# Kernel optimization log

Measured on AMD Instinct MI355X. Metric: run time of the kernel, lower is better.

## Reference

```python
import jax, jax.numpy as jnp
import numpy as np
from jax import lax

R = 4                 # radius (init kwarg)
EPS = 2.0             # eps (init kwarg)
K = 2 * R + 1         # stencil size


def _dir_kernels():
    """8 directional box kernels [8,1,K,K]: L,R,U,D,NW,NE,SW,SE (matches torch construction)."""
    base = np.ones((K, K), np.float32)
    L = base.copy(); L[:, R + 1:] = 0
    Rk = base.copy(); Rk[:, :R] = 0
    U = base.copy(); U[R + 1:, :] = 0
    D = base.copy(); D[:R, :] = 0
    NW = U.copy(); NE = U.copy(); SW = D.copy(); SE = D.copy()
    half = float((R + 1) * (2 * R + 1))
    L, Rk, U, D = L / half, Rk / half, U / half, D / half
    NW[:, R + 1:] = 0; NE[:, :R] = 0; SW[:, R + 1:] = 0; SE[:, :R] = 0
    quad = float((R + 1) ** 2)
    NW, NE, SW, SE = NW / quad, NE / quad, SW / quad, SE / quad
    return jnp.asarray(np.stack([L, Rk, U, D, NW, NE, SW, SE])[:, None])


def _pad(x):
    # ReplicationPad2d(R)
    return jnp.pad(x, ((0, 0), (0, 0), (R, R), (R, R)), mode='edge')


def _conv(x, w, groups=1):
    return lax.conv_general_dilated(
        x, w, window_strides=(1, 1), padding='VALID',
        dimension_numbers=('NCHW', 'OIHW', 'NCHW'), feature_group_count=groups)


def _resize_bilinear_ac(x, H, W):
    """Bilinear resize with align_corners=True, separable gather. x: [N,C,h,w]."""
    n, c, h, w = x.shape
    dt = x.dtype

    def coords(out, src):
        t = jnp.arange(out, dtype=dt) * (jnp.asarray(src - 1, dt) / jnp.asarray(out - 1, dt))
        i0 = jnp.clip(jnp.floor(t).astype(jnp.int32), 0, src - 2)
        f = t - i0.astype(dt)
        return i0, f

    y0, fy = coords(H, h)
    x0, fx = coords(W, w)
    rows = x[:, :, y0, :] * (1 - fy)[None, None, :, None] + x[:, :, y0 + 1, :] * fy[None, None, :, None]
    return rows[:, :, :, x0] * (1 - fx) + rows[:, :, :, x0 + 1] * fx


def setup_inputs() -> dict:
    key = jax.random.key(0)
    k1, k2, k3 = jax.random.split(key, 3)
    lr_x = jax.random.uniform(k1, (1, 3, 256, 256), jnp.float32) * 255.0
    lr_y = jax.random.uniform(k2, (1, 3, 256, 256), jnp.float32) * 255.0
    hr_x = jax.random.uniform(k3, (1, 3, 1024, 1024), jnp.float32) * 255.0
    box_w = jnp.full((3, 1, K, K), 1.0 / (K * K), jnp.float32)  # depthwise box filter weights
    return {"lr_x": lr_x, "lr_y": lr_y, "hr_x": hr_x, "box_w": box_w}


def reference(lr_x, lr_y, hr_x, box_w):
    H, W = hr_x.shape[2], hr_x.shape[3]
    box = lambda t: _conv(_pad(t), box_w, groups=3)

    # --- guided filter coefficients at low res ---
    mean_x = box(lr_x)
    mean_y = box(lr_y)
    cov_xy = box(lr_x * lr_y) - mean_x * mean_y
    var_x = box(lr_x * lr_x) - mean_x * mean_x
    A = cov_xy / (var_x + EPS)
    b = mean_y - A * mean_x

    # --- upsample A, b to hr (bilinear, align_corners=True) ---
    A = _resize_bilinear_ac(A, H, W)
    b = _resize_bilinear_ac(b, H, W)

    # --- 8-direction side-window stencil; channels treated as batch ---
    dirw = _dir_kernels()                      # [8,1,K,K]
    A3 = _pad(A.reshape(3, 1, H, W))
    b3 = _pad(b.reshape(3, 1, H, W))
    im3 = hr_x.reshape(3, 1, H, W)
    cA = _conv(A3, dirw)                       # [3,8,H,W]
    cB = _conv(b3, dirw)                       # [3,8,H,W]
    d = cA * im3 + cB - im3                    # [3,8,H,W]

    idx = jnp.argmin(jnp.abs(d), axis=1, keepdims=True)
    dm = jnp.take_along_axis(d, idx, axis=1)   # min-|delta| direction
    res = (dm + im3).reshape(1, 3, H, W)

    # res.int() truncates toward zero, then clamp(0,255), then float
    return jnp.clip(jnp.trunc(res), 0.0, 255.0)
```

## Files before the change

kernel.cpp:

```cpp
#include <hip/hip_runtime.h>

#define LRN 256
#define HRN 1024
#define SCALE (255.0f/1023.0f)

typedef float v2 __attribute__((ext_vector_type(2)));

#define WS_LUTW 4096
#define WS_AB   65536

__device__ inline int anchor_of(int u) {
    int k = min(max(u - 4, 0), HRN - 1);
    float t = (float)k * SCALE;
    int i = (int)t; if (i > LRN - 2) i = LRN - 2;
    return i;
}

__device__ inline float4 mkw(int k0, int k1, int a) {
    float4 w = make_float4(0.f, 0.f, 0.f, 0.f);
    for (int k = k0; k <= k1; ++k) {
        int kc = min(max(k, 0), HRN - 1);
        float t = (float)kc * SCALE;
        int i = (int)t; if (i > LRN - 2) i = LRN - 2;
        float f = t - (float)i;
        int off = i - a;
        float wa = 1.0f - f, wb = f;
        w.x += (off == 0) ? wa : 0.0f;
        w.y += (off == 1) ? wa : ((off == 0) ? wb : 0.0f);
        w.z += (off == 2) ? wa : ((off == 1) ? wb : 0.0f);
        w.w += (off == 2) ? wb : 0.0f;
    }
    return w;
}

__global__ __launch_bounds__(256, 4) void lr_kernel(
    const float* __restrict__ lrx, const float* __restrict__ lry,
    float* __restrict__ ws)
{
    __shared__ float4 sV[24][40];
    __shared__ float4 sHS[24][32];

    const int c  = blockIdx.z;
    const int X0 = blockIdx.x * 32, Y0 = blockIdx.y * 16;
    const int tid = threadIdx.y * 32 + threadIdx.x;
    const float* px = lrx + c * LRN * LRN;
    const float* py = lry + c * LRN * LRN;

    if (c == 0 && blockIdx.y == 0 && tid < 128) {
        int u = blockIdx.x * 128 + tid;
        int a = anchor_of(u);
        ((int*)ws)[u] = a;
        float4* w = (float4*)((char*)ws + WS_LUTW) + u * 3;
        w[0] = mkw(u - 4, u,     a);
        w[1] = mkw(u,     u + 4, a);
        w[2] = mkw(u - 4, u + 4, a);
    }

    for (int i = tid; i < 24 * 40; i += 256) {
        int r = i / 40, cc = i - r * 40;
        int gy = min(max(Y0 - 4 + r, 0), LRN - 1);
        int gx = min(max(X0 - 4 + cc, 0), LRN - 1);
        float xv = px[gy * LRN + gx];
        float yv = py[gy * LRN + gx];
        sV[r][cc] = make_float4(xv, yv, xv * yv, xv * xv);
    }
    __syncthreads();

    for (int i = tid; i < 24 * 32; i += 256) {
        int r = i / 32, cc = i & 31;
        float4 s = sV[r][cc];
        #pragma unroll
        for (int k = 1; k < 9; ++k) {
            float4 v = sV[r][cc + k];
            s.x += v.x; s.y += v.y; s.z += v.z; s.w += v.w;
        }
        sHS[r][cc] = s;
    }
    __syncthreads();

    v2* ab_out = (v2*)((char*)ws + WS_AB);
    for (int i = tid; i < 16 * 32; i += 256) {
        int r = i / 32, cc = i & 31;
        float4 s = sHS[r][cc];
        #pragma unroll
        for (int k = 1; k < 9; ++k) {
            float4 v = sHS[r + k][cc];
            s.x += v.x; s.y += v.y; s.z += v.z; s.w += v.w;
        }
        const float inv81 = 1.0f / 81.0f;
        float mx = s.x * inv81, my = s.y * inv81;
        float cov = s.z * inv81 - mx * my;
        float var = s.w * inv81 - mx * mx;
        float A = cov / (var + 2.0f);
        float B = my - A * mx;
        v2 ab; ab.x = A; ab.y = B;
        ab_out[(c * LRN + (Y0 + r)) * LRN + X0 + cc] = ab;
    }
}

#define TX 64
#define TYV 32
#define WROWS 8
#define LRC 20
#define LRR 12

__global__ __launch_bounds__(256, 6) void hr_kernel(
    const float* __restrict__ hrx, const float* __restrict__ ws,
    float* __restrict__ out)
{
    __shared__ v2     sHL[LRR][TX];
    __shared__ v2     sHR[LRR][TX];
    __shared__ v2     sHF[LRR][TX];
    __shared__ v2     sAB[LRR][LRC];
    __shared__ float4 sXW[TX][3];
    __shared__ int    sXA[TX];
    __shared__ float4 sYW[TYV][3];
    __shared__ int    sYA[TYV];

    const int c  = blockIdx.z;
    const int X0 = blockIdx.x * TX, Y0 = blockIdx.y * TYV;
    const int tid = threadIdx.y * TX + threadIdx.x;

    const int*    lutA = (const int*)ws;
    const float4* lutW = (const float4*)((const char*)ws + WS_LUTW);
    const v2*     AB   = (const v2*)((const char*)ws + WS_AB) + c * LRN * LRN;

    const int rowbase = lutA[Y0];
    const int colbase = lutA[X0];

    if (tid < TX) {
        int u = X0 + tid;
        sXA[tid] = lutA[u] - colbase;
        sXW[tid][0] = lutW[u * 3 + 0];
        sXW[tid][1] = lutW[u * 3 + 1];
        sXW[tid][2] = lutW[u * 3 + 2];
    } else if (tid < TX + TYV) {
        int r = tid - TX, u = Y0 + r;
        sYA[r] = lutA[u] - rowbase;
        sYW[r][0] = lutW[u * 3 + 0];
        sYW[r][1] = lutW[u * 3 + 1];
        sYW[r][2] = lutW[u * 3 + 2];
    }
    for (int i = tid; i < LRR * LRC; i += 256) {
        int r = i / LRC, cc = i - r * LRC;
        int gy = min(rowbase + r, LRN - 1);
        int gx = min(colbase + cc, LRN - 1);
        sAB[r][cc] = AB[gy * LRN + gx];
    }
    __syncthreads();

    for (int i = tid; i < LRR * TX; i += 256) {
        int r = i >> 6, x = i & 63;
        int c0 = sXA[x];
        float4 wL = sXW[x][0], wR = sXW[x][1], wF = sXW[x][2];
        v2 a0 = sAB[r][c0],     a1 = sAB[r][c0 + 1];
        v2 a2 = sAB[r][c0 + 2], a3 = sAB[r][c0 + 3];
        v2 hl, hr_, hf;
        hl  = a0 * wL.x;
        hl  = __builtin_elementwise_fma((v2)(wL.y), a1, hl);
        hl  = __builtin_elementwise_fma((v2)(wL.z), a2, hl);
        hl  = __builtin_elementwise_fma((v2)(wL.w), a3, hl);
        hr_ = a0 * wR.x;
        hr_ = __builtin_elementwise_fma((v2)(wR.y), a1, hr_);
        hr_ = __builtin_elementwise_fma((v2)(wR.z), a2, hr_);
        hr_ = __builtin_elementwise_fma((v2)(wR.w), a3, hr_);
        hf  = a0 * wF.x;
        hf  = __builtin_elementwise_fma((v2)(wF.y), a1, hf);
        hf  = __builtin_elementwise_fma((v2)(wF.z), a2, hf);
        hf  = __builtin_elementwise_fma((v2)(wF.w), a3, hf);
        sHL[r][x] = hl; sHR[r][x] = hr_; sHF[r][x] = hf;
    }
    __syncthreads();

    const int tx = threadIdx.x, tyw = threadIdx.y;
    const int row0 = tyw * WROWS;
    const float i45 = 1.0f / 45.0f, i25 = 1.0f / 25.0f;
    const float* hp = hrx + (c * HRN + Y0 + row0) * HRN + X0 + tx;
    float*       op = out + (c * HRN + Y0 + row0) * HRN + X0 + tx;

    int rap = sYA[row0];
    v2 hL0 = sHL[rap][tx],     hL1 = sHL[rap + 1][tx];
    v2 hL2 = sHL[rap + 2][tx], hL3 = sHL[rap + 3][tx];
    v2 hR0 = sHR[rap][tx],     hR1 = sHR[rap + 1][tx];
    v2 hR2 = sHR[rap + 2][tx], hR3 = sHR[rap + 3][tx];
    v2 hF0 = sHF[rap][tx],     hF1 = sHF[rap + 1][tx];
    v2 hF2 = sHF[rap + 2][tx], hF3 = sHF[rap + 3][tx];

    #pragma unroll
    for (int j = 0; j < WROWS; ++j) {
        const int yr = row0 + j;
        const int ra = sYA[yr];
        if (ra != rap) {
            hL0 = hL1; hL1 = hL2; hL2 = hL3; hL3 = sHL[ra + 3][tx];
            hR0 = hR1; hR1 = hR2; hR2 = hR3; hR3 = sHR[ra + 3][tx];
            hF0 = hF1; hF1 = hF2; hF2 = hF3; hF3 = sHF[ra + 3][tx];
            rap = ra;
        }
        const float4 wT = sYW[yr][0], wB = sYW[yr][1], wFv = sYW[yr][2];

        v2 aL = 0, aR = 0, aU = 0, aD = 0;
        v2 aNW = 0, aNE = 0, aSW = 0, aSE = 0;
        #define TAPK(WT, WB, WF, HL, HR_, HF)                         \
            aU  = __builtin_elementwise_fma((v2)(WT), HF,  aU);       \
            aD  = __builtin_elementwise_fma((v2)(WB), HF,  aD);       \
            aL  = __builtin_elementwise_fma((v2)(WF), HL,  aL);       \
            aR  = __builtin_elementwise_fma((v2)(WF), HR_, aR);       \
            aNW = __builtin_elementwise_fma((v2)(WT), HL,  aNW);      \
            aNE = __builtin_elementwise_fma((v2)(WT), HR_, aNE);      \
            aSW = __builtin_elementwise_fma((v2)(WB), HL,  aSW);      \
            aSE = __builtin_elementwise_fma((v2)(WB), HR_, aSE);
        TAPK(wT.x, wB.x, wFv.x, hL0, hR0, hF0)
        TAPK(wT.y, wB.y, wFv.y, hL1, hR1, hF1)
        TAPK(wT.z, wB.z, wFv.z, hL2, hR2, hF2)
        TAPK(wT.w, wB.w, wFv.w, hL3, hR3, hF3)
        #undef TAPK

        float xv = hp[j * HRN];

        float d0 = fmaf(i45, fmaf(aL.x,  xv, aL.y),  -xv);
        float d1 = fmaf(i45, fmaf(aR.x,  xv, aR.y),  -xv);
        float d2 = fmaf(i45, fmaf(aU.x,  xv, aU.y),  -xv);
        float d3 = fmaf(i45, fmaf(aD.x,  xv, aD.y),  -xv);
        float d4 = fmaf(i25, fmaf(aNW.x, xv, aNW.y), -xv);
        float d5 = fmaf(i25, fmaf(aNE.x, xv, aNE.y), -xv);
        float d6 = fmaf(i25, fmaf(aSW.x, xv, aSW.y), -xv);
        float d7 = fmaf(i25, fmaf(aSE.x, xv, aSE.y), -xv);

        float a0 = fabsf(d0), a1 = fabsf(d1), a2 = fabsf(d2), a3 = fabsf(d3);
        float a4 = fabsf(d4), a5 = fabsf(d5), a6 = fabsf(d6), a7 = fabsf(d7);
        bool c01 = a0 <= a1; float w01 = c01 ? d0 : d1; float m01 = c01 ? a0 : a1;
        bool c23 = a2 <= a3; float w23 = c23 ? d2 : d3; float m23 = c23 ? a2 : a3;
        bool c45 = a4 <= a5; float w45 = c45 ? d4 : d5; float m45 = c45 ? a4 : a5;
        bool c67 = a6 <= a7; float w67 = c67 ? d6 : d7; float m67 = c67 ? a6 : a7;
        bool cA_ = m01 <= m23; float wA = cA_ ? w01 : w23; float mA = cA_ ? m01 : m23;
        bool cB_ = m45 <= m67; float wB_ = cB_ ? w45 : w67; float mB = cB_ ? m45 : m67;
        float bd = (mA <= mB) ? wA : wB_;

        float res = __builtin_amdgcn_fmed3f(truncf(bd + xv), 0.0f, 255.0f);
        op[j * HRN] = res;
    }
}

extern "C" void kernel_launch(void* const* d_in, const int* in_sizes, int n_in,
                              void* d_out, int out_size, void* d_ws, size_t ws_size,
                              hipStream_t stream) {
    const float* lrx = (const float*)d_in[0];
    const float* lry = (const float*)d_in[1];
    const float* hrx = (const float*)d_in[2];
    (void)d_in[3]; (void)in_sizes; (void)n_in; (void)out_size; (void)ws_size;

    float* ws   = (float*)d_ws;
    float* outp = (float*)d_out;

    lr_kernel<<<dim3(LRN / 32, LRN / 16, 3), dim3(32, 8), 0, stream>>>(lrx, lry, ws);
    hr_kernel<<<dim3(HRN / TX, HRN / TYV, 3), dim3(TX, 4), 0, stream>>>(hrx, ws, outp);
}
```

Measured before the change: 87.90 us.

## Fuse low-res coefficient kernel into high-res kernel, recomputing A,b per tile

Merges the low-resolution box-filter/coefficient kernel into the high-resolution stencil kernel. Each HR block now recomputes the A,b patch it needs (with halo) from lr_x/lr_y in shared memory and computes its interpolation weight LUTs inline instead of reading them from workspace. This removes a kernel launch, the global round trip of A,b and the LUT, and the dependency between the two launches. The cost is redundant low-res box-filter work across overlapping tiles, and more shared memory and instructions per block, which may affect occupancy.

```diff
diff --git a/kernel.cpp b/kernel.cpp
--- a/kernel.cpp
+++ b/kernel.cpp
@@ -6,8 +6,13 @@
 
 typedef float v2 __attribute__((ext_vector_type(2)));
 
-#define WS_LUTW 4096
-#define WS_AB   65536
+#define TX 64
+#define TYV 32
+#define WROWS 8
+#define LRC 20
+#define LRR 12
+#define GC (LRC + 8)
+#define GR (LRR + 8)
 
 __device__ inline int anchor_of(int u) {
     int k = min(max(u - 4, 0), HRN - 1);
@@ -33,41 +38,61 @@
     return w;
 }
 
-__global__ __launch_bounds__(256, 4) void lr_kernel(
+__global__ __launch_bounds__(256, 6) void fused_kernel(
     const float* __restrict__ lrx, const float* __restrict__ lry,
-    float* __restrict__ ws)
+    const float* __restrict__ hrx, float* __restrict__ out)
 {
-    __shared__ float4 sV[24][40];
-    __shared__ float4 sHS[24][32];
+    __shared__ alignas(16) char region1[18432];
+    float4 (*sV)[GC]   = reinterpret_cast<float4(*)[GC]>(region1);
+    float4 (*sHS)[LRC] = reinterpret_cast<float4(*)[LRC]>(region1 + GR * GC * 16);
+    v2 (*sHL)[TX] = reinterpret_cast<v2(*)[TX]>(region1);
+    v2 (*sHR)[TX] = reinterpret_cast<v2(*)[TX]>(region1 + 6144);
+    v2 (*sHF)[TX] = reinterpret_cast<v2(*)[TX]>(region1 + 12288);
+
+    __shared__ v2     sAB[LRR][LRC];
+    __shared__ float4 sXWL[TX], sXWR[TX], sXWF[TX];
+    __shared__ int    sXA[TX];
+    __shared__ float4 sYWT[TYV], sYWB[TYV], sYWF[TYV];
+    __shared__ int    sYA[TYV];
 
     const int c  = blockIdx.z;
-    const int X0 = blockIdx.x * 32, Y0 = blockIdx.y * 16;
-    const int tid = threadIdx.y * 32 + threadIdx.x;
+    const int X0 = blockIdx.x * TX, Y0 = blockIdx.y * TYV;
+    const int tid = threadIdx.y * TX + threadIdx.x;
     const float* px = lrx + c * LRN * LRN;
     const float* py = lry + c * LRN * LRN;
 
-    if (c == 0 && blockIdx.y == 0 && tid < 128) {
-        int u = blockIdx.x * 128 + tid;
-        int a = anchor_of(u);
-        ((int*)ws)[u] = a;
-        float4* w = (float4*)((char*)ws + WS_LUTW) + u * 3;
-        w[0] = mkw(u - 4, u,     a);
-        w[1] = mkw(u,     u + 4, a);
-        w[2] = mkw(u - 4, u + 4, a);
-    }
-
-    for (int i = tid; i < 24 * 40; i += 256) {
-        int r = i / 40, cc = i - r * 40;
-        int gy = min(max(Y0 - 4 + r, 0), LRN - 1);
-        int gx = min(max(X0 - 4 + cc, 0), LRN - 1);
+    const int rowbase = anchor_of(Y0);
+    const int colbase = anchor_of(X0);
+
+    if (tid < TX) {
+        int x = X0 + tid;
+        int a = anchor_of(x);
+        sXA[tid] = a - colbase;
+        sXWL[tid] = mkw(x - 4, x,     a);
+        sXWR[tid] = mkw(x,     x + 4, a);
+        sXWF[tid] = mkw(x - 4, x + 4, a);
+    } else if (tid < TX + TYV) {
+        int r = tid - TX;
+        int y = Y0 + r;
+        int a = anchor_of(y);
+        sYA[r] = a - rowbase;
+        sYWT[r] = mkw(y - 4, y,     a);
+        sYWB[r] = mkw(y,     y + 4, a);
+        sYWF[r] = mkw(y - 4, y + 4, a);
+    }
+
+    for (int i = tid; i < GR * GC; i += 256) {
+        int r = i / GC, cc = i - r * GC;
+        int gy = min(max(rowbase - 4 + r, 0), LRN - 1);
+        int gx = min(max(colbase - 4 + cc, 0), LRN - 1);
         float xv = px[gy * LRN + gx];
         float yv = py[gy * LRN + gx];
         sV[r][cc] = make_float4(xv, yv, xv * yv, xv * xv);
     }
     __syncthreads();
 
-    for (int i = tid; i < 24 * 32; i += 256) {
-        int r = i / 32, cc = i & 31;
+    for (int i = tid; i < GR * LRC; i += 256) {
+        int r = i / LRC, cc = i - r * LRC;
         float4 s = sV[r][cc];
         #pragma unroll
         for (int k = 1; k < 9; ++k) {
@@ -78,9 +103,8 @@
     }
     __syncthreads();
 
-    v2* ab_out = (v2*)((char*)ws + WS_AB);
-    for (int i = tid; i < 16 * 32; i += 256) {
-        int r = i / 32, cc = i & 31;
+    for (int i = tid; i < LRR * LRC; i += 256) {
+        int r = i / LRC, cc = i - r * LRC;
         float4 s = sHS[r][cc];
         #pragma unroll
         for (int k = 1; k < 9; ++k) {
@@ -94,65 +118,14 @@
         float A = cov / (var + 2.0f);
         float B = my - A * mx;
         v2 ab; ab.x = A; ab.y = B;
-        ab_out[(c * LRN + (Y0 + r)) * LRN + X0 + cc] = ab;
-    }
-}
-
-#define TX 64
-#define TYV 32
-#define WROWS 8
-#define LRC 20
-#define LRR 12
-
-__global__ __launch_bounds__(256, 6) void hr_kernel(
-    const float* __restrict__ hrx, const float* __restrict__ ws,
-    float* __restrict__ out)
-{
-    __shared__ v2     sHL[LRR][TX];
-    __shared__ v2     sHR[LRR][TX];
-    __shared__ v2     sHF[LRR][TX];
-    __shared__ v2     sAB[LRR][LRC];
-    __shared__ float4 sXW[TX][3];
-    __shared__ int    sXA[TX];
-    __shared__ float4 sYW[TYV][3];
-    __shared__ int    sYA[TYV];
-
-    const int c  = blockIdx.z;
-    const int X0 = blockIdx.x * TX, Y0 = blockIdx.y * TYV;
-    const int tid = threadIdx.y * TX + threadIdx.x;
-
-    const int*    lutA = (const int*)ws;
-    const float4* lutW = (const float4*)((const char*)ws + WS_LUTW);
-    const v2*     AB   = (const v2*)((const char*)ws + WS_AB) + c * LRN * LRN;
-
-    const int rowbase = lutA[Y0];
-    const int colbase = lutA[X0];
-
-    if (tid < TX) {
-        int u = X0 + tid;
-        sXA[tid] = lutA[u] - colbase;
-        sXW[tid][0] = lutW[u * 3 + 0];
-        sXW[tid][1] = lutW[u * 3 + 1];
-        sXW[tid][2] = lutW[u * 3 + 2];
-    } else if (tid < TX + TYV) {
-        int r = tid - TX, u = Y0 + r;
-        sYA[r] = lutA[u] - rowbase;
-        sYW[r][0] = lutW[u * 3 + 0];
-        sYW[r][1] = lutW[u * 3 + 1];
-        sYW[r][2] = lutW[u * 3 + 2];
-    }
-    for (int i = tid; i < LRR * LRC; i += 256) {
-        int r = i / LRC, cc = i - r * LRC;
-        int gy = min(rowbase + r, LRN - 1);
-        int gx = min(colbase + cc, LRN - 1);
-        sAB[r][cc] = AB[gy * LRN + gx];
+        sAB[r][cc] = ab;
     }
     __syncthreads();
 
     for (int i = tid; i < LRR * TX; i += 256) {
         int r = i >> 6, x = i & 63;
         int c0 = sXA[x];
-        float4 wL = sXW[x][0], wR = sXW[x][1], wF = sXW[x][2];
+        float4 wL = sXWL[x], wR = sXWR[x], wF = sXWF[x];
         v2 a0 = sAB[r][c0],     a1 = sAB[r][c0 + 1];
         v2 a2 = sAB[r][c0 + 2], a3 = sAB[r][c0 + 3];
         v2 hl, hr_, hf;
@@ -196,7 +169,7 @@
             hF0 = hF1; hF1 = hF2; hF2 = hF3; hF3 = sHF[ra + 3][tx];
             rap = ra;
         }
-        const float4 wT = sYW[yr][0], wB = sYW[yr][1], wFv = sYW[yr][2];
+        const float4 wT = sYWT[yr], wB = sYWB[yr], wFv = sYWF[yr];
 
         v2 aL = 0, aR = 0, aU = 0, aD = 0;
         v2 aNW = 0, aNE = 0, aSW = 0, aSE = 0;
@@ -247,11 +220,9 @@
     const float* lrx = (const float*)d_in[0];
     const float* lry = (const float*)d_in[1];
     const float* hrx = (const float*)d_in[2];
-    (void)d_in[3]; (void)in_sizes; (void)n_in; (void)out_size; (void)ws_size;
-
-    float* ws   = (float*)d_ws;
+    (void)d_in[3]; (void)in_sizes; (void)n_in; (void)out_size;
+    (void)d_ws; (void)ws_size;
+
     float* outp = (float*)d_out;
-
-    lr_kernel<<<dim3(LRN / 32, LRN / 16, 3), dim3(32, 8), 0, stream>>>(lrx, lry, ws);
-    hr_kernel<<<dim3(HRN / TX, HRN / TYV, 3), dim3(TX, 4), 0, stream>>>(hrx, ws, outp);
-}
+    fused_kernel<<<dim3(HRN / TX, HRN / TYV, 3), dim3(TX, 4), 0, stream>>>(lrx, lry, hrx, outp);
+}
```

After: 83.53 us. -5.0%, faster.
